# Kernel optimization log

Measured on AMD Instinct MI355X. Metric: run time of the kernel, lower is better.

Reference implementation:

```python
import jax, jax.numpy as jnp
import numpy as np
from jax import lax

STRIDE = 1
PADDING = 1


def setup_inputs() -> dict:
    key = jax.random.key(0)
    kx, kw = jax.random.split(key)
    x = jax.random.normal(kx, (32, 64, 64, 64), dtype=jnp.float32)
    # weights are angles uniform on (-pi, pi)
    weight = jax.random.uniform(kw, (128, 64, 3, 3), dtype=jnp.float32,
                                minval=-jnp.pi, maxval=jnp.pi)
    return {"x": x, "weight": weight}


def _ring_conv2d(x, weight, stride, padding):
    # out[b,o,i,j] = sum_{c,kh,kw} cos(x_pad[b,c,i*s+kh,j*s+kw] - w[o,c,kh,kw])
    # cos(a-b) = cos a cos b + sin a sin b  ->  two standard convolutions.
    # Pad the raw angles with zeros first (a padded zero contributes cos(-w)).
    p = padding
    xp = jnp.pad(x, ((0, 0), (0, 0), (p, p), (p, p)))
    dn = ('NCHW', 'OIHW', 'NCHW')
    out = lax.conv_general_dilated(jnp.cos(xp), jnp.cos(weight),
                                   window_strides=(stride, stride),
                                   padding='VALID', dimension_numbers=dn)
    out = out + lax.conv_general_dilated(jnp.sin(xp), jnp.sin(weight),
                                         window_strides=(stride, stride),
                                         padding='VALID', dimension_numbers=dn)
    return out


def reference(x, weight):
    return _ring_conv2d(x, weight, STRIDE, PADDING)
```

## Files before the change

### kernel.cpp

```cpp
#include <hip/hip_runtime.h>
#include <hip/hip_bf16.h>


typedef _Float16 half8 __attribute__((ext_vector_type(8)));
typedef float f32x16 __attribute__((ext_vector_type(16)));

#define NB 32
#define NC 64
#define NH 64
#define NW 64
#define NO 128
#define PW 66
#define PSTRIDE 72
#define TROWS 10
#define TCOLS 34
#define TPX (TROWS * TCOLS)

union U16 { unsigned short u; _Float16 h; };
union HB { uint4 u4; unsigned long long q[2]; half8 h; };

__device__ inline unsigned pack_cs(float ang) {
    float s, c;
    sincosf(ang, &s, &c);
    U16 uc, us; uc.h = (_Float16)c; us.h = (_Float16)s;
    return (unsigned)uc.u | ((unsigned)us.u << 16);
}

__device__ inline unsigned pack_cs_fast(float ang) {
    float s, c;
    __sincosf(ang, &s, &c);
    U16 uc, us; uc.h = (_Float16)c; us.h = (_Float16)s;
    return (unsigned)uc.u | ((unsigned)us.u << 16);
}

__global__ __launch_bounds__(256) void prep_all(const float* __restrict__ x,
                                                const float* __restrict__ w,
                                                uint4* __restrict__ xp,
                                                uint4* __restrict__ wqa) {
    __shared__ unsigned ls[64 * 65];
    const int blk = blockIdx.x;
    const int t = threadIdx.x;

    if (blk < NB * NH) {
        const int b = blk >> 6, row = blk & 63;
#pragma unroll
        for (int pass = 0; pass < 16; ++pass) {
            int c = pass * 4 + (t >> 6);
            int col = t & 63;
            float v = x[((size_t)(b * NC + c) * NH + row) * NW + col];
            ls[c * 65 + col] = pack_cs_fast(v);
        }
        __syncthreads();
        const int q = t & 3, col = t >> 2;
#pragma unroll
        for (int cg = 0; cg < 4; ++cg) {
            uint4 vv;
            vv.x = ls[(cg * 16 + 4 * q + 0) * 65 + col];
            vv.y = ls[(cg * 16 + 4 * q + 1) * 65 + col];
            vv.z = ls[(cg * 16 + 4 * q + 2) * 65 + col];
            vv.w = ls[(cg * 16 + 4 * q + 3) * 65 + col];
            xp[(size_t)(((b * 4 + cg) * PW + row + 1) * PW + col + 1) * 4 + q] = vv;
        }
    } else if (blk < NB * NH + 72) {
        int tt = (blk - NB * NH) * 256 + t;
        if (tt < 36 * 2 * 128 * 2) {
            int g2 = tt & 1, o = (tt >> 1) & 127, kk = (tt >> 8) & 1, chunk = tt >> 9;
            int cg = chunk / 9, kpos = chunk % 9, kh = kpos / 3, kw = kpos % 3;
            unsigned r[4];
#pragma unroll
            for (int m = 0; m < 4; ++m) {
                int c = cg * 16 + kk * 8 + g2 * 4 + m;
                float ang = w[((o * NC + c) * 3 + kh) * 3 + kw];
                r[m] = pack_cs(ang);
            }
            wqa[tt] = make_uint4(r[0], r[1], r[2], r[3]);
        }
    } else {
        const int bc = blk - NB * NH - 72;
        uint4* base = xp + (size_t)bc * PW * PW * 4;
        const uint4 v = make_uint4(0x3C00u, 0x3C00u, 0x3C00u, 0x3C00u);
        for (int idx = t; idx < 260 * 4; idx += 256) {
            int p = idx >> 2, q = idx & 3;
            int r, c;
            if (p < 66)       { r = 0;       c = p; }
            else if (p < 132) { r = 65;      c = p - 66; }
            else if (p < 196) { r = p - 131; c = 0; }
            else              { r = p - 195; c = 65; }
            base[(size_t)(r * PW + c) * 4 + q] = v;
        }
    }
}

__global__ __launch_bounds__(256, 2) void ring_conv(const uint4* __restrict__ xp,
                                                    const uint4* __restrict__ wqa,
                                                    float* __restrict__ out) {
    __shared__ __align__(16) char xs[TPX * PSTRIDE];

    const int d = blockIdx.x;
    const int blk = (d & 7) * 64 + (d >> 3);

    const int ch = blk & 1, rq = (blk >> 1) & 7, b = blk >> 4;
    const int row0 = rq * 8, col0 = ch * 32;

    const int t = threadIdx.x, lane = t & 63, wid = t >> 6;
    const int l31 = lane & 31, g2 = lane >> 5;
    const int op = wid & 1, rg = wid >> 1;
    const int rowbase = rg * 4;

    f32x16 acc[2][4] = {};

    int goff[6], loff[6];
#pragma unroll
    for (int k = 0; k < 6; ++k) {
        int e = k * 256 + t;
        if (e > TPX * 4 - 1) e = TPX * 4 - 1;
        int p = e >> 2, q = e & 3;
        int rr = p / TCOLS, cc = p - rr * TCOLS;
        goff[k] = ((row0 + rr) * PW + (col0 + cc)) * 4 + q;
        loff[k] = p * PSTRIDE + q * 16;
    }
    const size_t img_stride = (size_t)PW * PW * 4;
    const uint4* img0 = xp + (size_t)(b * 4) * img_stride;

    const int xlane = l31 * PSTRIDE + g2 * 16;
    const uint4* wbase = wqa + (op * 64 + l31) * 2 + g2;

    {
        uint4 S[6];
#pragma unroll
        for (int k = 0; k < 6; ++k) S[k] = img0[goff[k]];
#pragma unroll
        for (int k = 0; k < 6; ++k) {
            char* dst = xs + loff[k];
            *(unsigned long long*)dst = (unsigned long long)S[k].x | ((unsigned long long)S[k].y << 32);
            *(unsigned long long*)(dst + 8) = (unsigned long long)S[k].z | ((unsigned long long)S[k].w << 32);
        }
    }
    __syncthreads();

    for (int cg = 0; cg < 4; ++cg) {
        const uint4* wa = wbase + (size_t)(cg * 18) * 256;

        HB Ar[4][2];
#pragma unroll
        for (int i = 0; i < 4; ++i) {
            Ar[i][0].u4 = wa[i * 256];
            Ar[i][1].u4 = wa[i * 256 + 64];
        }
        HB Bop[2][4];
#pragma unroll
        for (int r = 0; r < 4; ++r) {
            const char* sp = xs + (rowbase + r) * TCOLS * PSTRIDE + xlane;
            Bop[0][r].q[0] = *(const unsigned long long*)sp;
            Bop[0][r].q[1] = *(const unsigned long long*)(sp + 8);
        }

        uint4 S[6];
        if (cg < 3) {
            const uint4* img = img0 + (size_t)(cg + 1) * img_stride;
#pragma unroll
            for (int k = 0; k < 6; ++k) S[k] = img[goff[k]];
        }

#pragma unroll
        for (int s = 0; s < 18; ++s) {
            const int cp = s & 1, np = cp ^ 1;
            if (s < 17) {
                const int s1 = s + 1, kp1 = s1 >> 1, kk1 = s1 & 1;
                const int kh1 = kp1 / 3, kw1 = kp1 % 3;
#pragma unroll
                for (int r = 0; r < 4; ++r) {
                    const char* sp = xs
                        + (((rowbase + r + kh1) * TCOLS + kw1) * PSTRIDE + kk1 * 32) + xlane;
                    Bop[np][r].q[0] = *(const unsigned long long*)sp;
                    Bop[np][r].q[1] = *(const unsigned long long*)(sp + 8);
                }
            }
            __builtin_amdgcn_s_setprio(1);
#pragma unroll
            for (int r = 0; r < 4; ++r)
#pragma unroll
                for (int f = 0; f < 2; ++f)
                    acc[f][r] = __builtin_amdgcn_mfma_f32_32x32x16_f16(
                        Ar[s & 3][f].h, Bop[cp][r].h, acc[f][r], 0, 0, 0);
            __builtin_amdgcn_s_setprio(0);
            if (s < 14) {
                Ar[s & 3][0].u4 = wa[(s + 4) * 256];
                Ar[s & 3][1].u4 = wa[(s + 4) * 256 + 64];
            }
        }

        __syncthreads();
        if (cg < 3) {
#pragma unroll
            for (int k = 0; k < 6; ++k) {
                char* dst = xs + loff[k];
                *(unsigned long long*)dst = (unsigned long long)S[k].x | ((unsigned long long)S[k].y << 32);
                *(unsigned long long*)(dst + 8) = (unsigned long long)S[k].z | ((unsigned long long)S[k].w << 32);
            }
            __syncthreads();
        }
    }

#pragma unroll
    for (int f = 0; f < 2; ++f)
#pragma unroll
        for (int r = 0; r < 4; ++r) {
            const int orow = row0 + rowbase + r;
#pragma unroll
            for (int reg = 0; reg < 16; ++reg) {
                int o = op * 64 + f * 32 + (reg & 3) + 8 * (reg >> 2) + 4 * g2;
                out[(((size_t)b * NO + o) * NH + orow) * NW + col0 + l31] = acc[f][r][reg];
            }
        }
}

extern "C" void kernel_launch(void* const* d_in, const int* in_sizes, int n_in,
                              void* d_out, int out_size, void* d_ws, size_t ws_size,
                              hipStream_t stream) {
    const float* x = (const float*)d_in[0];
    const float* w = (const float*)d_in[1];

    uint4* xpnt = (uint4*)d_ws;
    uint4* wqp = (uint4*)((char*)d_ws + (size_t)36 * 1024 * 1024);

    prep_all<<<NB * NH + 72 + 128, 256, 0, stream>>>(x, w, xpnt, wqp);
    ring_conv<<<512, 256, 0, stream>>>(xpnt, wqp, (float*)d_out);
}
```

Baseline: 57.26 us.

## Fuse input sincos packing and padding into conv kernel, drop intermediate buffer

The conv kernel now reads raw fp32 x directly, computes the cos/sin fp16 pair per element in-register, and handles the padding border with a validity mask. This removes the prep pass that wrote a padded, packed copy of x to workspace and the extra global round trip that came with it. In exchange, each block recomputes sincos for its halo-overlapping tile (about 22 elements per thread per channel group). It also issues many scalar 4-byte loads and LDS writes instead of 16-byte ones, which raises register pressure and VALU work inside the MFMA loop.

New measurement: 65.62 us. 1.15x slower.

```diff
diff --git a/kernel.cpp b/kernel.cpp
--- a/kernel.cpp
+++ b/kernel.cpp
@@ -15,6 +15,8 @@
 #define TROWS 10
 #define TCOLS 34
 #define TPX (TROWS * TCOLS)
+#define NELEM (TPX * 16)
+#define NPASS 22
 
 union U16 { unsigned short u; _Float16 h; };
 union HB { uint4 u4; unsigned long long q[2]; half8 h; };
@@ -33,65 +35,23 @@
     return (unsigned)uc.u | ((unsigned)us.u << 16);
 }
 
-__global__ __launch_bounds__(256) void prep_all(const float* __restrict__ x,
-                                                const float* __restrict__ w,
-                                                uint4* __restrict__ xp,
-                                                uint4* __restrict__ wqa) {
-    __shared__ unsigned ls[64 * 65];
-    const int blk = blockIdx.x;
-    const int t = threadIdx.x;
-
-    if (blk < NB * NH) {
-        const int b = blk >> 6, row = blk & 63;
+__global__ __launch_bounds__(256) void prep_w(const float* __restrict__ w,
+                                              uint4* __restrict__ wqa) {
+    int tt = blockIdx.x * 256 + threadIdx.x;
+    if (tt >= 36 * 2 * 128 * 2) return;
+    int g2 = tt & 1, o = (tt >> 1) & 127, kk = (tt >> 8) & 1, chunk = tt >> 9;
+    int cg = chunk / 9, kpos = chunk % 9, kh = kpos / 3, kw = kpos % 3;
+    unsigned r[4];
 #pragma unroll
-        for (int pass = 0; pass < 16; ++pass) {
-            int c = pass * 4 + (t >> 6);
-            int col = t & 63;
-            float v = x[((size_t)(b * NC + c) * NH + row) * NW + col];
-            ls[c * 65 + col] = pack_cs_fast(v);
-        }
-        __syncthreads();
-        const int q = t & 3, col = t >> 2;
-#pragma unroll
-        for (int cg = 0; cg < 4; ++cg) {
-            uint4 vv;
-            vv.x = ls[(cg * 16 + 4 * q + 0) * 65 + col];
-            vv.y = ls[(cg * 16 + 4 * q + 1) * 65 + col];
-            vv.z = ls[(cg * 16 + 4 * q + 2) * 65 + col];
-            vv.w = ls[(cg * 16 + 4 * q + 3) * 65 + col];
-            xp[(size_t)(((b * 4 + cg) * PW + row + 1) * PW + col + 1) * 4 + q] = vv;
-        }
-    } else if (blk < NB * NH + 72) {
-        int tt = (blk - NB * NH) * 256 + t;
-        if (tt < 36 * 2 * 128 * 2) {
-            int g2 = tt & 1, o = (tt >> 1) & 127, kk = (tt >> 8) & 1, chunk = tt >> 9;
-            int cg = chunk / 9, kpos = chunk % 9, kh = kpos / 3, kw = kpos % 3;
-            unsigned r[4];
-#pragma unroll
-            for (int m = 0; m < 4; ++m) {
-                int c = cg * 16 + kk * 8 + g2 * 4 + m;
-                float ang = w[((o * NC + c) * 3 + kh) * 3 + kw];
-                r[m] = pack_cs(ang);
-            }
-            wqa[tt] = make_uint4(r[0], r[1], r[2], r[3]);
-        }
-    } else {
-        const int bc = blk - NB * NH - 72;
-        uint4* base = xp + (size_t)bc * PW * PW * 4;
-        const uint4 v = make_uint4(0x3C00u, 0x3C00u, 0x3C00u, 0x3C00u);
-        for (int idx = t; idx < 260 * 4; idx += 256) {
-            int p = idx >> 2, q = idx & 3;
-            int r, c;
-            if (p < 66)       { r = 0;       c = p; }
-            else if (p < 132) { r = 65;      c = p - 66; }
-            else if (p < 196) { r = p - 131; c = 0; }
-            else              { r = p - 195; c = 65; }
-            base[(size_t)(r * PW + c) * 4 + q] = v;
-        }
+    for (int m = 0; m < 4; ++m) {
+        int c = cg * 16 + kk * 8 + g2 * 4 + m;
+        float ang = w[((o * NC + c) * 3 + kh) * 3 + kw];
+        r[m] = pack_cs(ang);
     }
+    wqa[tt] = make_uint4(r[0], r[1], r[2], r[3]);
 }
 
-__global__ __launch_bounds__(256, 2) void ring_conv(const uint4* __restrict__ xp,
+__global__ __launch_bounds__(256, 2) void ring_conv(const float* __restrict__ xr,
                                                     const uint4* __restrict__ wqa,
                                                     float* __restrict__ out) {
     __shared__ __align__(16) char xs[TPX * PSTRIDE];
@@ -99,8 +59,8 @@
     const int d = blockIdx.x;
     const int blk = (d & 7) * 64 + (d >> 3);
 
-    const int ch = blk & 1, rq = (blk >> 1) & 7, b = blk >> 4;
-    const int row0 = rq * 8, col0 = ch * 32;
+    const int ch2 = blk & 1, rq = (blk >> 1) & 7, b = blk >> 4;
+    const int row0 = rq * 8, col0 = ch2 * 32;
 
     const int t = threadIdx.x, lane = t & 63, wid = t >> 6;
     const int l31 = lane & 31, g2 = lane >> 5;
@@ -109,33 +69,53 @@
 
     f32x16 acc[2][4] = {};
 
-    int goff[6], loff[6];
-#pragma unroll
-    for (int k = 0; k < 6; ++k) {
-        int e = k * 256 + t;
-        if (e > TPX * 4 - 1) e = TPX * 4 - 1;
-        int p = e >> 2, q = e & 3;
-        int rr = p / TCOLS, cc = p - rr * TCOLS;
-        goff[k] = ((row0 + rr) * PW + (col0 + cc)) * 4 + q;
-        loff[k] = p * PSTRIDE + q * 16;
-    }
-    const size_t img_stride = (size_t)PW * PW * 4;
-    const uint4* img0 = xp + (size_t)(b * 4) * img_stride;
-
+    const float* xb = xr + (size_t)b * NC * NH * NW;
     const int xlane = l31 * PSTRIDE + g2 * 16;
     const uint4* wbase = wqa + (op * 64 + l31) * 2 + g2;
 
-    {
-        uint4 S[6];
+    unsigned vmask = 0;
 #pragma unroll
-        for (int k = 0; k < 6; ++k) S[k] = img0[goff[k]];
-#pragma unroll
-        for (int k = 0; k < 6; ++k) {
-            char* dst = xs + loff[k];
-            *(unsigned long long*)dst = (unsigned long long)S[k].x | ((unsigned long long)S[k].y << 32);
-            *(unsigned long long*)(dst + 8) = (unsigned long long)S[k].z | ((unsigned long long)S[k].w << 32);
-        }
+    for (int k = 0; k < NPASS; ++k) {
+        int e = k * 256 + t; if (e > NELEM - 1) e = NELEM - 1;
+        int p = e % TPX;
+        int rr = p / TCOLS, cc = p - rr * TCOLS;
+        int gr = row0 - 1 + rr, gc = col0 - 1 + cc;
+        if (((unsigned)gr < 64u) && ((unsigned)gc < 64u)) vmask |= 1u << k;
     }
+
+    float S[NPASS];
+    unsigned pk[NPASS];
+
+#define STAGE_LOAD(cgi)                                                        \
+    {   const float* src = xb + (size_t)(cgi) * 16 * NH * NW;                  \
+        _Pragma("unroll")                                                      \
+        for (int k = 0; k < NPASS; ++k) {                                      \
+            int e = k * 256 + t; if (e > NELEM - 1) e = NELEM - 1;             \
+            int c16 = e / TPX, p = e - c16 * TPX;                              \
+            int rr = p / TCOLS, cc = p - rr * TCOLS;                           \
+            int gr = row0 - 1 + rr, gc = col0 - 1 + cc;                        \
+            gr = min(max(gr, 0), 63); gc = min(max(gc, 0), 63);                \
+            S[k] = src[(c16 * NH + gr) * NW + gc];                             \
+        } }
+
+#define STAGE_PACK()                                                           \
+    {   _Pragma("unroll")                                                      \
+        for (int k = 0; k < NPASS; ++k) {                                      \
+            float v = ((vmask >> k) & 1u) ? S[k] : 0.f;                        \
+            pk[k] = pack_cs_fast(v);                                           \
+        } }
+
+#define STAGE_WRITE()                                                          \
+    {   _Pragma("unroll")                                                      \
+        for (int k = 0; k < NPASS; ++k) {                                      \
+            int e = k * 256 + t; if (e > NELEM - 1) e = NELEM - 1;             \
+            int c16 = e / TPX, p = e - c16 * TPX;                              \
+            *(unsigned*)&xs[p * PSTRIDE + c16 * 4] = pk[k];                    \
+        } }
+
+    STAGE_LOAD(0)
+    STAGE_PACK()
+    STAGE_WRITE()
     __syncthreads();
 
     for (int cg = 0; cg < 4; ++cg) {
@@ -155,12 +135,7 @@
             Bop[0][r].q[1] = *(const unsigned long long*)(sp + 8);
         }
 
-        uint4 S[6];
-        if (cg < 3) {
-            const uint4* img = img0 + (size_t)(cg + 1) * img_stride;
-#pragma unroll
-            for (int k = 0; k < 6; ++k) S[k] = img[goff[k]];
-        }
+        if (cg < 3) STAGE_LOAD(cg + 1)
 
 #pragma unroll
         for (int s = 0; s < 18; ++s) {
@@ -190,14 +165,10 @@
             }
         }
 
-        __syncthreads();
         if (cg < 3) {
-#pragma unroll
-            for (int k = 0; k < 6; ++k) {
-                char* dst = xs + loff[k];
-                *(unsigned long long*)dst = (unsigned long long)S[k].x | ((unsigned long long)S[k].y << 32);
-                *(unsigned long long*)(dst + 8) = (unsigned long long)S[k].z | ((unsigned long long)S[k].w << 32);
-            }
+            STAGE_PACK()
+            __syncthreads();
+            STAGE_WRITE()
             __syncthreads();
         }
     }
@@ -221,9 +192,8 @@
     const float* x = (const float*)d_in[0];
     const float* w = (const float*)d_in[1];
 
-    uint4* xpnt = (uint4*)d_ws;
-    uint4* wqp = (uint4*)((char*)d_ws + (size_t)36 * 1024 * 1024);
+    uint4* wqp = (uint4*)d_ws;
 
-    prep_all<<<NB * NH + 72 + 128, 256, 0, stream>>>(x, w, xpnt, wqp);
-    ring_conv<<<512, 256, 0, stream>>>(xpnt, wqp, (float*)d_out);
+    prep_w<<<72, 256, 0, stream>>>(w, wqp);
+    ring_conv<<<512, 256, 0, stream>>>(x, wqp, (float*)d_out);
 }
```

## Stage input tiles via direct global-to-LDS loads with double buffering

Applied to the files above, without the earlier changes.

Replaces the register-staged global→LDS copy with global_load_lds 16-byte direct transfers into a double-buffered shared tile. The LDS layout changes from per-pixel padded rows to quad-major planes, which allows 128-bit ds_reads for B operands. Explicit vmcnt waits and s_barriers overlap the next channel group's load with the current MFMA loop. The gains would come from removing VGPR staging and the extra syncthreads. The costs are double the LDS footprint and a layout with no padding, which may cause bank conflicts.

Measured after the change: 58.64 us. 1.02x slower.

```diff
diff --git a/kernel.cpp b/kernel.cpp
--- a/kernel.cpp
+++ b/kernel.cpp
@@ -11,13 +11,13 @@
 #define NW 64
 #define NO 128
 #define PW 66
-#define PSTRIDE 72
 #define TROWS 10
 #define TCOLS 34
 #define TPX (TROWS * TCOLS)
+#define NLD (TPX * 4)
 
 union U16 { unsigned short u; _Float16 h; };
-union HB { uint4 u4; unsigned long long q[2]; half8 h; };
+union HB { uint4 u4; half8 h; };
 
 __device__ inline unsigned pack_cs(float ang) {
     float s, c;
@@ -91,16 +91,21 @@
     }
 }
 
+#define GLOAD16(gptr, ldsptr)                                                   \
+    __builtin_amdgcn_global_load_lds(                                           \
+        (const __attribute__((address_space(1))) unsigned*)(gptr),              \
+        (__attribute__((address_space(3))) unsigned*)(ldsptr), 16, 0, 0)
+
 __global__ __launch_bounds__(256, 2) void ring_conv(const uint4* __restrict__ xp,
                                                     const uint4* __restrict__ wqa,
                                                     float* __restrict__ out) {
-    __shared__ __align__(16) char xs[TPX * PSTRIDE];
+    __shared__ __align__(16) char xs[2][NLD * 16];
 
     const int d = blockIdx.x;
     const int blk = (d & 7) * 64 + (d >> 3);
 
-    const int ch = blk & 1, rq = (blk >> 1) & 7, b = blk >> 4;
-    const int row0 = rq * 8, col0 = ch * 32;
+    const int ch2 = blk & 1, rq = (blk >> 1) & 7, b = blk >> 4;
+    const int row0 = rq * 8, col0 = ch2 * 32;
 
     const int t = threadIdx.x, lane = t & 63, wid = t >> 6;
     const int l31 = lane & 31, g2 = lane >> 5;
@@ -109,36 +114,48 @@
 
     f32x16 acc[2][4] = {};
 
-    int goff[6], loff[6];
+    int goff[6];
 #pragma unroll
     for (int k = 0; k < 6; ++k) {
-        int e = k * 256 + t;
-        if (e > TPX * 4 - 1) e = TPX * 4 - 1;
-        int p = e >> 2, q = e & 3;
+        int e = wid * 340 + k * 64 + lane;
+        if (e > NLD - 1) e = NLD - 1;
+        int q = e / TPX, p = e - q * TPX;
         int rr = p / TCOLS, cc = p - rr * TCOLS;
         goff[k] = ((row0 + rr) * PW + (col0 + cc)) * 4 + q;
-        loff[k] = p * PSTRIDE + q * 16;
-    }
+    }
+    const int ebase = wid * 340;
     const size_t img_stride = (size_t)PW * PW * 4;
     const uint4* img0 = xp + (size_t)(b * 4) * img_stride;
 
-    const int xlane = l31 * PSTRIDE + g2 * 16;
+#define STAGE(bufi, cgi)                                                        \
+    {   const uint4* img = img0 + (size_t)(cgi) * img_stride;                   \
+        _Pragma("unroll")                                                       \
+        for (int k = 0; k < 5; ++k)                                             \
+            GLOAD16(img + goff[k], &xs[bufi][(ebase + k * 64) * 16]);           \
+        if (lane < 20) GLOAD16(img + goff[5], &xs[bufi][(ebase + 320) * 16]);   \
+    }
+
     const uint4* wbase = wqa + (op * 64 + l31) * 2 + g2;
 
-    {
-        uint4 S[6];
-#pragma unroll
-        for (int k = 0; k < 6; ++k) S[k] = img0[goff[k]];
-#pragma unroll
-        for (int k = 0; k < 6; ++k) {
-            char* dst = xs + loff[k];
-            *(unsigned long long*)dst = (unsigned long long)S[k].x | ((unsigned long long)S[k].y << 32);
-            *(unsigned long long*)(dst + 8) = (unsigned long long)S[k].z | ((unsigned long long)S[k].w << 32);
-        }
-    }
-    __syncthreads();
-
+    STAGE(0, 0)
+    asm volatile("s_waitcnt vmcnt(0)" ::: "memory");
+    __builtin_amdgcn_sched_barrier(0);
+    __builtin_amdgcn_s_barrier();
+
+#pragma unroll
     for (int cg = 0; cg < 4; ++cg) {
+        const int cur = cg & 1;
+
+        if (cg < 3) {
+            STAGE(cur ^ 1, cg + 1)
+            asm volatile("s_waitcnt vmcnt(6)" ::: "memory");
+        } else {
+            asm volatile("s_waitcnt vmcnt(0)" ::: "memory");
+        }
+        __builtin_amdgcn_sched_barrier(0);
+        __builtin_amdgcn_s_barrier();
+
+        const char* xbuf = xs[cur];
         const uint4* wa = wbase + (size_t)(cg * 18) * 256;
 
         HB Ar[4][2];
@@ -149,18 +166,9 @@
         }
         HB Bop[2][4];
 #pragma unroll
-        for (int r = 0; r < 4; ++r) {
-            const char* sp = xs + (rowbase + r) * TCOLS * PSTRIDE + xlane;
-            Bop[0][r].q[0] = *(const unsigned long long*)sp;
-            Bop[0][r].q[1] = *(const unsigned long long*)(sp + 8);
-        }
-
-        uint4 S[6];
-        if (cg < 3) {
-            const uint4* img = img0 + (size_t)(cg + 1) * img_stride;
-#pragma unroll
-            for (int k = 0; k < 6; ++k) S[k] = img[goff[k]];
-        }
+        for (int r = 0; r < 4; ++r)
+            Bop[0][r].u4 = *(const uint4*)(xbuf
+                + ((size_t)(g2 * TPX + (rowbase + r) * TCOLS + l31)) * 16);
 
 #pragma unroll
         for (int s = 0; s < 18; ++s) {
@@ -169,12 +177,10 @@
                 const int s1 = s + 1, kp1 = s1 >> 1, kk1 = s1 & 1;
                 const int kh1 = kp1 / 3, kw1 = kp1 % 3;
 #pragma unroll
-                for (int r = 0; r < 4; ++r) {
-                    const char* sp = xs
-                        + (((rowbase + r + kh1) * TCOLS + kw1) * PSTRIDE + kk1 * 32) + xlane;
-                    Bop[np][r].q[0] = *(const unsigned long long*)sp;
-                    Bop[np][r].q[1] = *(const unsigned long long*)(sp + 8);
-                }
+                for (int r = 0; r < 4; ++r)
+                    Bop[np][r].u4 = *(const uint4*)(xbuf
+                        + ((size_t)((2 * kk1 + g2) * TPX
+                                    + (rowbase + r + kh1) * TCOLS + l31 + kw1)) * 16);
             }
             __builtin_amdgcn_s_setprio(1);
 #pragma unroll
@@ -190,16 +196,7 @@
             }
         }
 
-        __syncthreads();
-        if (cg < 3) {
-#pragma unroll
-            for (int k = 0; k < 6; ++k) {
-                char* dst = xs + loff[k];
-                *(unsigned long long*)dst = (unsigned long long)S[k].x | ((unsigned long long)S[k].y << 32);
-                *(unsigned long long*)(dst + 8) = (unsigned long long)S[k].z | ((unsigned long long)S[k].w << 32);
-            }
-            __syncthreads();
-        }
+        __builtin_amdgcn_s_barrier();
     }
 
 #pragma unroll
```
